# Optimization experiments

Hardware: AMD Instinct MI355X
Metric: run time of the kernel (lower is better)

## Reference

```python
import jax, jax.numpy as jnp
import numpy as np
import math

D = 512; H = 4; HD = 128; S = 100; B = 32
HIN, WIN = 143, 111
HOUT, WOUT = 135, 103
FLAT = HIN * WIN  # 15873


def _pe():
    pos = np.arange(S, dtype=np.float32)[:, None]
    div = np.exp(np.arange(0, D, 2, dtype=np.float32) * (-math.log(10000.0) / D))
    pe = np.zeros((S, D), dtype=np.float32)
    pe[:, 0::2] = np.sin(pos * div)
    pe[:, 1::2] = np.cos(pos * div)
    return jnp.asarray(pe[:, None, :])  # (S,1,D)


def _pool_mat(n_in, n_out):
    # PyTorch AdaptiveAvgPool semantics: window [floor(i*in/out), ceil((i+1)*in/out))
    M = np.zeros((n_out, n_in), dtype=np.float32)
    for i in range(n_out):
        s = (i * n_in) // n_out
        e = -((-(i + 1) * n_in) // n_out)
        M[i, s:e] = 1.0 / (e - s)
    return jnp.asarray(M)


def _ln(x, g, b, eps=1e-5):
    m = jnp.mean(x, -1, keepdims=True)
    v = jnp.mean((x - m) ** 2, -1, keepdims=True)
    return (x - m) * jax.lax.rsqrt(v + eps) * g + b


def _mha(q_in, kv_in, qkv_w, qkv_b, pw, pb, key_pad):
    # q_in: (Sq,B,D), kv_in: (Sk,B,D); seq-first like nn.Transformer
    q = q_in @ qkv_w[:D].T + qkv_b[:D]
    k = kv_in @ qkv_w[D:2 * D].T + qkv_b[D:2 * D]
    v = kv_in @ qkv_w[2 * D:].T + qkv_b[2 * D:]
    Sq, Bb = q.shape[0], q.shape[1]
    Sk = k.shape[0]
    q = q.reshape(Sq, Bb, H, HD)
    k = k.reshape(Sk, Bb, H, HD)
    v = v.reshape(Sk, Bb, H, HD)
    sc = jnp.einsum('qbhd,kbhd->bhqk', q, k) / math.sqrt(HD)
    if key_pad is not None:
        sc = jnp.where(key_pad[:, None, None, :], -1e9, sc)
    a = jax.nn.softmax(sc, -1)
    o = jnp.einsum('bhqk,kbhd->qbhd', a, v).reshape(Sq, Bb, D)
    return o @ pw.T + pb


def _forward(x, fc1_w, fc1_b, fc2_w, fc2_b, fc3_w, fc3_b,
             out1_w, out1_b, out2_w, out2_b, out3_w, out3_b,
             enc_qkv_w, enc_qkv_b, enc_proj_w, enc_proj_b,
             enc_ff1_w, enc_ff1_b, enc_ff2_w, enc_ff2_b,
             enc_ln1_g, enc_ln1_b, enc_ln2_g, enc_ln2_b, enc_lnf_g, enc_lnf_b,
             dec_sa_qkv_w, dec_sa_qkv_b, dec_sa_proj_w, dec_sa_proj_b,
             dec_ca_qkv_w, dec_ca_qkv_b, dec_ca_proj_w, dec_ca_proj_b,
             dec_ff1_w, dec_ff1_b, dec_ff2_w, dec_ff2_b,
             dec_ln1_g, dec_ln1_b, dec_ln2_g, dec_ln2_b, dec_ln3_g, dec_ln3_b,
             dec_lnf_g, dec_lnf_b):
    Bb = x.shape[0]
    # Vectorized replacement of the per-sample torch.nonzero double loop:
    # padding[b,i] = True iff all timesteps k >= i are all-zero (and i >= 1).
    nz = jnp.any(x != 0, axis=(2, 3))  # (B,S)
    suffix_any = jnp.flip(jnp.cumsum(jnp.flip(nz, 1).astype(jnp.int32), 1), 1) > 0
    padding = (~suffix_any).at[:, 0].set(False)  # torch loop never touches step 0

    h = x.reshape(Bb * S, FLAT)
    h = jax.nn.relu(h @ fc1_w.T + fc1_b)
    h = jax.nn.relu(h @ fc2_w.T + fc2_b)
    h = jax.nn.relu(h @ fc3_w.T + fc3_b)
    h = h.reshape(Bb, S, D).transpose(1, 0, 2) + _pe()  # (S,B,D)

    for i in range(2):  # encoder, post-norm
        a = _mha(h, h, enc_qkv_w[i], enc_qkv_b[i], enc_proj_w[i], enc_proj_b[i], padding)
        h = _ln(h + a, enc_ln1_g[i], enc_ln1_b[i])
        f = jax.nn.relu(h @ enc_ff1_w[i].T + enc_ff1_b[i]) @ enc_ff2_w[i].T + enc_ff2_b[i]
        h = _ln(h + f, enc_ln2_g[i], enc_ln2_b[i])
    memory = _ln(h, enc_lnf_g, enc_lnf_b)

    t = jnp.ones((1, Bb, D), jnp.float32)  # trg
    for i in range(2):  # decoder, post-norm
        a = _mha(t, t, dec_sa_qkv_w[i], dec_sa_qkv_b[i], dec_sa_proj_w[i], dec_sa_proj_b[i], None)
        t = _ln(t + a, dec_ln1_g[i], dec_ln1_b[i])
        a = _mha(t, memory, dec_ca_qkv_w[i], dec_ca_qkv_b[i], dec_ca_proj_w[i], dec_ca_proj_b[i], None)
        t = _ln(t + a, dec_ln2_g[i], dec_ln2_b[i])
        f = jax.nn.relu(t @ dec_ff1_w[i].T + dec_ff1_b[i]) @ dec_ff2_w[i].T + dec_ff2_b[i]
        t = _ln(t + f, dec_ln3_g[i], dec_ln3_b[i])
    t = _ln(t, dec_lnf_g, dec_lnf_b)

    o = t[0]  # (B,512)
    o = jax.nn.relu(o @ out1_w.T + out1_b)
    o = jax.nn.relu(o @ out2_w.T + out2_b)
    o = jax.nn.relu(o @ out3_w.T + out3_b)
    o = o.reshape(Bb, HIN, WIN)
    return jnp.einsum('oh,bhw,pw->bop', _pool_mat(HIN, HOUT), o, _pool_mat(WIN, WOUT))


def setup_inputs() -> dict:
    key = jax.random.key(0)
    it = iter(jax.random.split(key, 48))

    def w(shape):
        return jax.random.normal(next(it), shape, jnp.float32) * 0.02

    x = jax.random.normal(next(it), (B, S, HIN, WIN), jnp.float32)
    lengths = jax.random.randint(next(it), (B,), 1, S + 1)
    keep = (jnp.arange(S)[None, :] < lengths[:, None]).astype(jnp.float32)
    x = x * keep[:, :, None, None]  # ragged: trailing timesteps are all-zero

    z, o1 = jnp.zeros, jnp.ones
    return dict(
        x=x,
        fc1_w=w((4096, FLAT)), fc1_b=z(4096),
        fc2_w=w((2048, 4096)), fc2_b=z(2048),
        fc3_w=w((D, 2048)), fc3_b=z(D),
        out1_w=w((2048, D)), out1_b=z(2048),
        out2_w=w((4096, 2048)), out2_b=z(4096),
        out3_w=w((FLAT, 4096)), out3_b=z(FLAT),
        enc_qkv_w=w((2, 3 * D, D)), enc_qkv_b=z((2, 3 * D)),
        enc_proj_w=w((2, D, D)), enc_proj_b=z((2, D)),
        enc_ff1_w=w((2, 1024, D)), enc_ff1_b=z((2, 1024)),
        enc_ff2_w=w((2, D, 1024)), enc_ff2_b=z((2, D)),
        enc_ln1_g=o1((2, D)), enc_ln1_b=z((2, D)),
        enc_ln2_g=o1((2, D)), enc_ln2_b=z((2, D)),
        enc_lnf_g=o1(D), enc_lnf_b=z(D),
        dec_sa_qkv_w=w((2, 3 * D, D)), dec_sa_qkv_b=z((2, 3 * D)),
        dec_sa_proj_w=w((2, D, D)), dec_sa_proj_b=z((2, D)),
        dec_ca_qkv_w=w((2, 3 * D, D)), dec_ca_qkv_b=z((2, 3 * D)),
        dec_ca_proj_w=w((2, D, D)), dec_ca_proj_b=z((2, D)),
        dec_ff1_w=w((2, 1024, D)), dec_ff1_b=z((2, 1024)),
        dec_ff2_w=w((2, D, 1024)), dec_ff2_b=z((2, D)),
        dec_ln1_g=o1((2, D)), dec_ln1_b=z((2, D)),
        dec_ln2_g=o1((2, D)), dec_ln2_b=z((2, D)),
        dec_ln3_g=o1((2, D)), dec_ln3_b=z((2, D)),
        dec_lnf_g=o1(D), dec_lnf_b=z(D),
    )


def reference(x, fc1_w, fc1_b, fc2_w, fc2_b, fc3_w, fc3_b,
              out1_w, out1_b, out2_w, out2_b, out3_w, out3_b,
              enc_qkv_w, enc_qkv_b, enc_proj_w, enc_proj_b,
              enc_ff1_w, enc_ff1_b, enc_ff2_w, enc_ff2_b,
              enc_ln1_g, enc_ln1_b, enc_ln2_g, enc_ln2_b, enc_lnf_g, enc_lnf_b,
              dec_sa_qkv_w, dec_sa_qkv_b, dec_sa_proj_w, dec_sa_proj_b,
              dec_ca_qkv_w, dec_ca_qkv_b, dec_ca_proj_w, dec_ca_proj_b,
              dec_ff1_w, dec_ff1_b, dec_ff2_w, dec_ff2_b,
              dec_ln1_g, dec_ln1_b, dec_ln2_g, dec_ln2_b, dec_ln3_g, dec_ln3_b,
              dec_lnf_g, dec_lnf_b):
    return _forward(x, fc1_w, fc1_b, fc2_w, fc2_b, fc3_w, fc3_b,
                    out1_w, out1_b, out2_w, out2_b, out3_w, out3_b,
                    enc_qkv_w, enc_qkv_b, enc_proj_w, enc_proj_b,
                    enc_ff1_w, enc_ff1_b, enc_ff2_w, enc_ff2_b,
                    enc_ln1_g, enc_ln1_b, enc_ln2_g, enc_ln2_b, enc_lnf_g, enc_lnf_b,
                    dec_sa_qkv_w, dec_sa_qkv_b, dec_sa_proj_w, dec_sa_proj_b,
                    dec_ca_qkv_w, dec_ca_qkv_b, dec_ca_proj_w, dec_ca_proj_b,
                    dec_ff1_w, dec_ff1_b, dec_ff2_w, dec_ff2_b,
                    dec_ln1_g, dec_ln1_b, dec_ln2_g, dec_ln2_b, dec_ln3_g, dec_ln3_b,
                    dec_lnf_g, dec_lnf_b)
```

## Files before the change

kernel.cpp:

```cpp
#include <hip/hip_runtime.h>
#include <hip/hip_bf16.h>

#define SEQ   100
#define BATCH 32
#define FLATIN 15873
#define KPAD1  16384
#define ROWS   3200
#define MPAD   3328
#define NOUT3  16000

typedef __attribute__((ext_vector_type(8))) short short8;
typedef __attribute__((ext_vector_type(4))) short short4v;
typedef __attribute__((ext_vector_type(4))) float f32x4;

__device__ __forceinline__ void gload_lds16(const void* g, void* l) {
  __builtin_amdgcn_global_load_lds((const __attribute__((address_space(1))) void*)g,
                                   (__attribute__((address_space(3))) void*)l, 16, 0, 0);
}

__device__ __forceinline__ int xcd_swizzle(int id, int nwg) {
  const int q = nwg >> 3, r = nwg & 7;
  const int x = id & 7, p = id >> 3;
  return (x < r ? x * (q + 1) : r * (q + 1) + (x - r) * q) + p;
}
// ... 86 lines not shown
__global__ __launch_bounds__(256)
void gemm_direct(const __hip_bfloat16* __restrict__ A, const __hip_bfloat16* __restrict__ W,
                 const float* __restrict__ bias, float* __restrict__ Cf,
                 __hip_bfloat16* __restrict__ Cb, int K, int ldc, int mtiles)
{
  __shared__ __align__(16) short lds[16384];
  short* As = lds;
  short* Bs = lds + 8192;
  const int GATHER = 0;
  const int* idx = nullptr;
  const int wg = xcd_swizzle(blockIdx.x, gridDim.x);
  const int m0 = (wg % mtiles) << 7;
  const int n0 = (wg / mtiles) << 7;

  GEMM_BODY(0, K)

  const int fr = lane & 15, fq = lane >> 4;
#pragma unroll
  for (int j = 0; j < 4; ++j) {
    const int n = n0 + wc + (j << 4) + fr;
    const float bb = bias[n];
#pragma unroll
    for (int i = 0; i < 4; ++i)
#pragma unroll
      for (int r = 0; r < 4; ++r) {
        const int m = m0 + wr + (i << 4) + (fq << 2) + r;
        float v = acc[i][j][r] + bb;
        if (RELU) v = fmaxf(v, 0.f);
        if (OF32) Cf[(size_t)m * ldc + n] = v;
        if (OB16) Cb[(size_t)m * ldc + n] = __float2bfloat16(v);
      }
  }
}

template<int RELU, int OF32, int OB16>
__global__ __launch_bounds__(256)
void reduce_kernel(const float* __restrict__ P, size_t pstride, int ksl,
                   const float* __restrict__ bias, float* __restrict__ Cf,
                   __hip_bfloat16* __restrict__ Cb, int N,
                   const int* __restrict__ cnt)
{
  const int row = blockIdx.y;
  if (cnt) { const int cp = (cnt[0] + 127) & ~127; if (row >= cp) return; }
  const int n = (blockIdx.x * 256 + threadIdx.x) * 4;
  if (n >= N) return;
  const size_t o = (size_t)row * N + n;
  const float4 b4 = *(const float4*)(bias + n);
  float4 s = *(const float4*)(P + o);
  for (int k = 1; k < ksl; ++k) {
    const float4 p = *(const float4*)(P + (size_t)k * pstride + o);
    s.x += p.x; s.y += p.y; s.z += p.z; s.w += p.w;
  }
  s.x += b4.x; s.y += b4.y; s.z += b4.z; s.w += b4.w;
  if (RELU) {
    s.x = fmaxf(s.x, 0.f); s.y = fmaxf(s.y, 0.f);
    s.z = fmaxf(s.z, 0.f); s.w = fmaxf(s.w, 0.f);
  }
  if (OF32) *(float4*)(Cf + o) = s;
  if (OB16) {
    union { short4v v; __hip_bfloat16 h[4]; } u;
    u.h[0] = __float2bfloat16(s.x);
    u.h[1] = __float2bfloat16(s.y);
    u.h[2] = __float2bfloat16(s.z);
    u.h[3] = __float2bfloat16(s.w);
    *(short4v*)(Cb + o) = u.v;
  }
}

__global__ __launch_bounds__(256)
void conv_x_kernel(const float* __restrict__ x, __hip_bfloat16* __restrict__ xb,
                   int* __restrict__ nz)
{
  __shared__ int sred[4];
  const int m = blockIdx.x;
  const int t = threadIdx.x;
  __hip_bfloat16* dst = xb + (size_t)m * KPAD1;
  if (m == ROWS) {
    const __hip_bfloat162 z2 = {__float2bfloat16(0.f), __float2bfloat16(0.f)};
    for (int c = t; c < (KPAD1 >> 1); c += 256) *(__hip_bfloat162*)(dst + 2 * c) = z2;
    return;
  }
  const float* src = x + (size_t)m * FLATIN;
  int any = 0;
  for (int c = t; c < FLATIN; c += 256) any |= (src[c] != 0.f);
  any = __any(any) ? 1 : 0;
  if ((t & 63) == 0) sred[t >> 6] = any;
  __syncthreads();
  const int ba = sred[0] | sred[1] | sred[2] | sred[3];
  if (t == 0) nz[m] = ba;
  if (!ba) return;
  for (int c = t; c < (KPAD1 >> 1); c += 256) {
    const int c0 = 2 * c;
    const float v0 = (c0 < FLATIN) ? src[c0] : 0.f;
    const float v1 = (c0 + 1 < FLATIN) ? src[c0 + 1] : 0.f;
    __hip_bfloat162 pr;
    pr.x = __float2bfloat16(v0);
    pr.y = __float2bfloat16(v1);
    *(__hip_bfloat162*)(dst + c0) = pr;
  }
}

__global__ __launch_bounds__(256)
void compact_kernel(const int* __restrict__ nz, int* __restrict__ idx,
                    int* __restrict__ pos, int* __restrict__ cnt,
                    int* __restrict__ pad)
{
  __shared__ int wsum[4];
  __shared__ int total;
  const int t = threadIdx.x;
  int loc[13];
  int c = 0;
#pragma unroll
  for (int i = 0; i < 13; ++i) {
    const int m = t * 13 + i;
    loc[i] = (m < ROWS) ? nz[m] : 0;
    c += loc[i];
  }
  int v = c;
#pragma unroll
  for (int o = 1; o < 64; o <<= 1) {
    const int u = __shfl_up(v, o);
    if ((t & 63) >= o) v += u;
  }
  if ((t & 63) == 63) wsum[t >> 6] = v;
  __syncthreads();
  int wbase = 0;
  for (int w = 0; w < (t >> 6); ++w) wbase += wsum[w];
  int p = wbase + v - c;
#pragma unroll
  for (int i = 0; i < 13; ++i) {
    const int m = t * 13 + i;
    if (m < ROWS) {
      if (loc[i]) { idx[p] = m; pos[m] = p; ++p; }
      else pos[m] = -1;
    }
  }
  if (t == 255) total = p;
  __syncthreads();
  const int count = total;
  if (t == 0) cnt[0] = count + 1;
  for (int i = count + t; i < MPAD; i += 256) idx[i] = ROWS;
  for (int m = t; m < ROWS; m += 256) if (pos[m] < 0) pos[m] = count;
  if (t < 32) {
    int any = 0;
    for (int s = 99; s >= 0; --s) {
      any |= nz[t * 100 + s];
      pad[t * 100 + s] = (s > 0 && !any) ? 1 : 0;
    }
  }
}

__global__ __launch_bounds__(256)
void cvt_pad_kernel(const float* __restrict__ in, __hip_bfloat16* __restrict__ out,
                    int rin, int cin, int cout)
{
  const int c = (blockIdx.x * 256 + threadIdx.x) * 2;
  const int r = blockIdx.y;
  if (c >= cout) return;
  const int rv = (r < rin);
  const float v0 = (rv && c < cin) ? in[(size_t)r * cin + c] : 0.f;
  const float v1 = (rv && c + 1 < cin) ? in[(size_t)r * cin + c + 1] : 0.f;
  __hip_bfloat162 pr;
  pr.x = __float2bfloat16(v0);
  pr.y = __float2bfloat16(v1);
  *(__hip_bfloat162*)(out + (size_t)r * cout + c) = pr;
}

struct CvtArgs {
  const float* src[8];
  __hip_bfloat16* dst[8];
  int cum[8];
};
__global__ __launch_bounds__(256)
void cvt_multi_kernel(CvtArgs a)
{
  const int bid = blockIdx.x;
  int seg = 0;
#pragma unroll
  for (int i = 1; i < 8; ++i) if (bid >= a.cum[i]) seg = i;
  const size_t e0 = ((size_t)(bid - a.cum[seg]) << 11) + (threadIdx.x << 3);
  const float4 v0 = *(const float4*)(a.src[seg] + e0);
  const float4 v1 = *(const float4*)(a.src[seg] + e0 + 4);
  union { short4v v; __hip_bfloat16 h[4]; } u0, u1;
  u0.h[0] = __float2bfloat16(v0.x); u0.h[1] = __float2bfloat16(v0.y);
  u0.h[2] = __float2bfloat16(v0.z); u0.h[3] = __float2bfloat16(v0.w);
  u1.h[0] = __float2bfloat16(v1.x); u1.h[1] = __float2bfloat16(v1.y);
  u1.h[2] = __float2bfloat16(v1.z); u1.h[3] = __float2bfloat16(v1.w);
  *(short4v*)(a.dst[seg] + e0) = u0.v;
  *(short4v*)(a.dst[seg] + e0 + 4) = u1.v;
}

struct TrArgs {
  const float* src[13];
  float* dst[13];
  int R[13], C[13], cum[13];
};
__global__ __launch_bounds__(256)
void transpose_kernel(TrArgs a)
{
  __shared__ float tbuf[64][65];
  const int bid = blockIdx.x;
  int seg = 0;
#pragma unroll
  for (int i = 1; i < 13; ++i) if (bid >= a.cum[i]) seg = i;
  const int local = bid - a.cum[seg];
  const int R = a.R[seg], C = a.C[seg];
  const int tilesC = C >> 6;
  const int r0 = (local / tilesC) << 6;
  const int c0 = (local % tilesC) << 6;
  const int tx = threadIdx.x & 63, ty = threadIdx.x >> 6;
  const float* s = a.src[seg];
  float* d = a.dst[seg];
#pragma unroll
  for (int i = 0; i < 16; ++i) {
    const int rr = (ty << 4) + i;
    tbuf[rr][tx] = s[(size_t)(r0 + rr) * C + c0 + tx];
  }
  __syncthreads();
#pragma unroll
  for (int i = 0; i < 16; ++i) {
    const int cc = (ty << 4) + i;
    d[(size_t)(c0 + cc) * R + r0 + tx] = tbuf[tx][cc];
  }
}

__global__ void bias_pad_kernel(const float* __restrict__ b, float* __restrict__ bp)
{
  const int i = blockIdx.x * 256 + threadIdx.x;
  if (i < NOUT3) bp[i] = (i < FLATIN) ? b[i] : 0.f;
}

__global__ __launch_bounds__(256)
void scatter_pe_reduce(const float* __restrict__ P, size_t pstride, int ksl,
                       const int* __restrict__ pos, const float* __restrict__ bias,
                       float* __restrict__ hf, __hip_bfloat16* __restrict__ hb)
{
  const int m = blockIdx.x;
  const int s = m % 100, b = m / 100;
  const int src = pos[m];
  const int t = threadIdx.x;
  const size_t sb = (size_t)src * 512;
  const size_t db = (size_t)(s * 32 + b) * 512;
#pragma unroll
  for (int u = 0; u < 2; ++u) {
    const int d = t + u * 256;
    float v = bias[d];
    for (int k = 0; k < ksl; ++k) v += P[(size_t)k * pstride + sb + d];
    const float div = expf((float)(2 * (d >> 1)) * (-9.210340371976184f / 512.f));
    const float arg = (float)s * div;
    const float pe = (d & 1) ? cosf(arg) : sinf(arg);
    v = fmaxf(v, 0.f) + pe;
    hf[db + d] = v;
    hb[db + d] = __float2bfloat16(v);
  }
}

__global__ __launch_bounds__(256)
void ln_kernel(const float* __restrict__ x, const float* __restrict__ res,
               const float* __restrict__ g, const float* __restrict__ bta,
               const float* __restrict__ gf, const float* __restrict__ bf_,
               int dofinal, float* __restrict__ y, __hip_bfloat16* __restrict__ yb)
{
  __shared__ float rs[4], rss[4];
  const int row = blockIdx.x;
  const int t = threadIdx.x;
  const size_t base = (size_t)row * 512;
  float v0 = x[base + t];
  float v1 = x[base + t + 256];
  if (res) { v0 += res[base + t]; v1 += res[base + t + 256]; }
  float o0, o1;
#pragma unroll
  for (int pass = 0; pass < 2; ++pass) {
    float s = v0 + v1, ss = v0 * v0 + v1 * v1;
#pragma unroll
    for (int o = 32; o > 0; o >>= 1) { s += __shfl_xor(s, o); ss += __shfl_xor(ss, o); }
    if ((t & 63) == 0) { rs[t >> 6] = s; rss[t >> 6] = ss; }
    __syncthreads();
    s = rs[0] + rs[1] + rs[2] + rs[3];
    ss = rss[0] + rss[1] + rss[2] + rss[3];
    __syncthreads();
    const float mean = s * (1.f / 512.f);
    const float var = ss * (1.f / 512.f) - mean * mean;
    const float inv = rsqrtf(var + 1e-5f);
    const float* gg = (pass == 0) ? g : gf;
    const float* bb = (pass == 0) ? bta : bf_;
    o0 = (v0 - mean) * inv * gg[t] + bb[t];
    o1 = (v1 - mean) * inv * gg[t + 256] + bb[t + 256];
    if (pass == 1 || !dofinal) break;
    v0 = o0; v1 = o1;
  }
  if (y) {
    y[base + t] = o0;
    y[base + t + 256] = o1;
  }
  if (yb) {
    yb[base + t] = __float2bfloat16(o0);
    yb[base + t + 256] = __float2bfloat16(o1);
  }
}

__global__ __launch_bounds__(256)
void enc_attn_kernel(const float* __restrict__ qkv, const int* __restrict__ pad,
                     __hip_bfloat16* __restrict__ ob)
{
  __shared__ float Ks[100][129];
  __shared__ float Qs[128];
  __shared__ float Ps[100];
  __shared__ float red[4];
  const int bh = blockIdx.x;
  const int b = bh >> 2, h = bh & 3;
  const int q0 = blockIdx.y * 25;
  const int t = threadIdx.x;
// ... 16 lines not shown
      for (int d = 0; d < 128; ++d) a += Qs[d] * kr[d];
      sc = masked ? -1e9f : (a * scale);
    }
    float mx = sc;
#pragma unroll
    for (int o = 32; o > 0; o >>= 1) mx = fmaxf(mx, __shfl_xor(mx, o));
    if ((t & 63) == 0) red[t >> 6] = mx;
    __syncthreads();
    mx = fmaxf(fmaxf(red[0], red[1]), fmaxf(red[2], red[3]));
    const float e = (t < 100) ? expf(sc - mx) : 0.f;
    float sm = e;
#pragma unroll
    for (int o = 32; o > 0; o >>= 1) sm += __shfl_xor(sm, o);
    __syncthreads();
    if ((t & 63) == 0) red[t >> 6] = sm;
    __syncthreads();
    sm = red[0] + red[1] + red[2] + red[3];
    if (t < 100) Ps[t] = e;
    __syncthreads();
    if (t < 128) {
      float a = 0.f;
      const float* vb = qkv + 1024 + h * 128 + t;
      for (int k = 0; k < 100; ++k) a += Ps[k] * vb[(size_t)(k * 32 + b) * 1536];
      ob[(size_t)(q * 32 + b) * 512 + h * 128 + t] = __float2bfloat16(a / sm);
    }
  }
}

template<int N, int K, int RELU>
__device__ __forceinline__ void gemvT(int tid, const float* S,
                                      const float* __restrict__ WT,
                                      const float* __restrict__ bias,
                                      float* out, float* part)
{
  constexpr int NQ = N / 4;
  constexpr int G = 512 / NQ;
  constexpr int KP = K / G;
  const int p = tid % NQ;
  const int g = tid / NQ;
  const float4* wp = (const float4*)WT;
  float ax = 0.f, ay = 0.f, az = 0.f, aw = 0.f;
  const int kend = g * KP + KP;
#pragma unroll 8
  for (int k = g * KP; k < kend; ++k) {
    const float s = S[k];
    const float4 w = wp[(size_t)k * NQ + p];
    ax += s * w.x; ay += s * w.y; az += s * w.z; aw += s * w.w;
  }
  float4 a4 = {ax, ay, az, aw};
  *(float4*)(part + g * N + 4 * p) = a4;
  __syncthreads();
#pragma unroll
  for (int n = tid; n < N; n += 512) {
    float v = bias[n];
#pragma unroll
    for (int q = 0; q < G; ++q) v += part[q * N + n];
    if (RELU) v = fmaxf(v, 0.f);
    out[n] = v;
  }
  __syncthreads();
}

#define BLOCK_LN512(V, G, B, O)                                                 \
  {                                                                             \
    float s_ = (V), ss_ = (V) * (V);                                            \
    _Pragma("unroll")                                                           \
    for (int o_ = 32; o_ > 0; o_ >>= 1) {                                       \
      s_ += __shfl_xor(s_, o_); ss_ += __shfl_xor(ss_, o_);                     \
    }                                                                           \
    if ((tid & 63) == 0) { red[tid >> 6] = s_; red2[tid >> 6] = ss_; }          \
    __syncthreads();                                                            \
    s_ = 0.f; ss_ = 0.f;                                                        \
    _Pragma("unroll")                                                           \
    for (int w_ = 0; w_ < 8; ++w_) { s_ += red[w_]; ss_ += red2[w_]; }          \
    const float mean_ = s_ * (1.f / 512.f);                                     \
    const float inv_ = rsqrtf(ss_ * (1.f / 512.f) - mean_ * mean_ + 1e-5f);     \
    O = ((V) - mean_) * inv_ * (G)[tid] + (B)[tid];                             \
    __syncthreads();                                                            \
  }

__global__ __launch_bounds__(512)
void dec_layer(const float* __restrict__ tin,
               const float* __restrict__ kvb,
               const float* __restrict__ WvT, const float* __restrict__ bv,
               const float* __restrict__ WpT, const float* __restrict__ bp,
               const float* __restrict__ g1, const float* __restrict__ b1,
               const float* __restrict__ WqT, const float* __restrict__ bq,
               const float* __restrict__ WcpT, const float* __restrict__ bcp,
               const float* __restrict__ g2, const float* __restrict__ b2,
               const float* __restrict__ W1T, const float* __restrict__ b1f,
               const float* __restrict__ W2T, const float* __restrict__ b2f,
               const float* __restrict__ g3, const float* __restrict__ b3,
               const float* __restrict__ gf, const float* __restrict__ bf_,
               int dofinal, float* __restrict__ tout)
{
  __shared__ float Ts[512], Bs[512], Cs[512], F1[1024], part[2048];
  __shared__ float Ps[4][104];
  __shared__ float red[8], red2[8];
  const int r = blockIdx.x, tid = threadIdx.x;
  Ts[tid] = tin ? tin[r * 512 + tid] : 1.0f;
  __syncthreads();

  gemvT<512, 512, 0>(tid, Ts, WvT, bv, Bs, part);
  gemvT<512, 512, 0>(tid, Bs, WpT, bp, Cs, part);
  {
    const float rr = Cs[tid] + Ts[tid];
    float o;
    BLOCK_LN512(rr, g1, b1, o)
    Ts[tid] = o;
  }
  __syncthreads();

  gemvT<512, 512, 0>(tid, Ts, WqT, bq, Bs, part);

  if (tid < 256) {
    const int h = tid >> 6, lane = tid & 63;
    const float scale = 0.08838834764831845f;
    const float* Qh = Bs + h * 128;
    float s0, s1 = -3e38f;
    {
      const float* kr = kvb + ((size_t)(lane * 32 + r)) * 1024 + h * 128;
      float a = 0.f;
#pragma unroll 16
      for (int d = 0; d < 128; ++d) a += Qh[d] * kr[d];
      s0 = a * scale;
    }
    if (lane + 64 < 100) {
      const float* kr = kvb + ((size_t)((lane + 64) * 32 + r)) * 1024 + h * 128;
      float a = 0.f;
#pragma unroll 16
      for (int d = 0; d < 128; ++d) a += Qh[d] * kr[d];
      s1 = a * scale;
    }
    float mx = fmaxf(s0, s1);
#pragma unroll
    for (int o = 32; o > 0; o >>= 1) mx = fmaxf(mx, __shfl_xor(mx, o));
    const float e0 = expf(s0 - mx);
    const float e1 = (lane + 64 < 100) ? expf(s1 - mx) : 0.f;
    float sm = e0 + e1;
#pragma unroll
    for (int o = 32; o > 0; o >>= 1) sm += __shfl_xor(sm, o);
    Ps[h][lane] = e0 / sm;
    if (lane + 64 < 100) Ps[h][lane + 64] = e1 / sm;
  }
  __syncthreads();
  if (tid < 256) {
    const int h = tid >> 6, lane = tid & 63;
#pragma unroll
    for (int u = 0; u < 2; ++u) {
      const int d = lane + u * 64;
      const float* vb = kvb + 512 + h * 128 + d;
      float a = 0.f;
      for (int k = 0; k < 100; ++k) a += Ps[h][k] * vb[(size_t)(k * 32 + r) * 1024];
      Bs[h * 128 + d] = a;
    }
  }
  __syncthreads();

  gemvT<512, 512, 0>(tid, Bs, WcpT, bcp, Cs, part);
  {
    const float rr = Cs[tid] + Ts[tid];
    float o;
    BLOCK_LN512(rr, g2, b2, o)
    Ts[tid] = o;
  }
  __syncthreads();

  gemvT<1024, 512, 1>(tid, Ts, W1T, b1f, F1, part);
  gemvT<512, 1024, 0>(tid, F1, W2T, b2f, Cs, part);
  {
    const float rr = Cs[tid] + Ts[tid];
    float o;
    BLOCK_LN512(rr, g3, b3, o)
    if (dofinal) {
      float f;
      BLOCK_LN512(o, gf, bf_, f)
      o = f;
    }
    tout[r * 512 + tid] = o;
  }
}

__global__ __launch_bounds__(256)
void out1_kernel(const float* __restrict__ A, const float* __restrict__ WT,
                 const float* __restrict__ bias, __hip_bfloat16* __restrict__ Cb)
{
  __shared__ float S[512];
  const int r = blockIdx.x;
  const int tid = threadIdx.x;
  const int n0 = tid * 8;
  if (r >= 32) {
    const short4v z = {0, 0, 0, 0};
    *(short4v*)(Cb + (size_t)r * 2048 + n0) = z;
    *(short4v*)(Cb + (size_t)r * 2048 + n0 + 4) = z;
    return;
  }
  S[tid] = A[r * 512 + tid];
  S[tid + 256] = A[r * 512 + tid + 256];
  __syncthreads();
  float a[8] = {0.f, 0.f, 0.f, 0.f, 0.f, 0.f, 0.f, 0.f};
  const float4* wp = (const float4*)WT;
#pragma unroll 4
  for (int k = 0; k < 512; ++k) {
    const float s = S[k];
    const float4 w0 = wp[(size_t)k * 512 + tid * 2];
    const float4 w1 = wp[(size_t)k * 512 + tid * 2 + 1];
    a[0] += s * w0.x; a[1] += s * w0.y; a[2] += s * w0.z; a[3] += s * w0.w;
    a[4] += s * w1.x; a[5] += s * w1.y; a[6] += s * w1.z; a[7] += s * w1.w;
  }
  union { short4v v; __hip_bfloat16 h[4]; } u0, u1;
#pragma unroll
  for (int i = 0; i < 4; ++i) {
    u0.h[i] = __float2bfloat16(fmaxf(a[i] + bias[n0 + i], 0.f));
    u1.h[i] = __float2bfloat16(fmaxf(a[4 + i] + bias[n0 + 4 + i], 0.f));
  }
  *(short4v*)(Cb + (size_t)r * 2048 + n0) = u0.v;
  *(short4v*)(Cb + (size_t)r * 2048 + n0 + 4) = u1.v;
}

__global__ __launch_bounds__(256)
void reduce_pool(const float* __restrict__ P, size_t pstride,
                 const float* __restrict__ bias, float* __restrict__ out)
{
  __shared__ float row[NOUT3];
  const int b = blockIdx.x, t = threadIdx.x;
  for (int n = t * 4; n < NOUT3; n += 1024) {
    const size_t o = (size_t)b * NOUT3 + n;
    float4 s = *(const float4*)(P + o);
#pragma unroll
    for (int k = 1; k < 4; ++k) {
      const float4 p = *(const float4*)(P + (size_t)k * pstride + o);
      s.x += p.x; s.y += p.y; s.z += p.z; s.w += p.w;
    }
    const float4 b4 = *(const float4*)(bias + n);
    row[n]     = fmaxf(s.x + b4.x, 0.f);
    row[n + 1] = fmaxf(s.y + b4.y, 0.f);
    row[n + 2] = fmaxf(s.z + b4.z, 0.f);
    row[n + 3] = fmaxf(s.w + b4.w, 0.f);
  }
  __syncthreads();
  for (int i = t; i < 135 * 103; i += 256) {
    const int j = i % 103, r = i / 103;
    const int rs = (r * 143) / 135, re = ((r + 1) * 143 + 134) / 135;
    const int cs = (j * 111) / 103, ce = ((j + 1) * 111 + 102) / 103;
    float s = 0.f;
    for (int rr = rs; rr < re; ++rr)
      for (int cc = cs; cc < ce; ++cc)
        s += row[rr * 111 + cc];
    out[(size_t)b * (135 * 103) + i] = s / (float)((re - rs) * (ce - cs));
  }
}

extern "C" void kernel_launch(void* const* d_in, const int* in_sizes, int n_in,
                              void* d_out, int out_size, void* d_ws, size_t ws_size,
                              hipStream_t stream)
{
  (void)in_sizes; (void)n_in; (void)out_size; (void)ws_size;

  const float* x          = (const float*)d_in[0];
  const float* fc1_w      = (const float*)d_in[1];
  const float* fc1_b      = (const float*)d_in[2];
  const float* fc2_w      = (const float*)d_in[3];
  const float* fc2_b      = (const float*)d_in[4];
  const float* fc3_w      = (const float*)d_in[5];
  const float* fc3_b      = (const float*)d_in[6];
  const float* out1_w     = (const float*)d_in[7];
  const float* out1_b     = (const float*)d_in[8];
  const float* out2_w     = (const float*)d_in[9];
  const float* out2_b     = (const float*)d_in[10];
  const float* out3_w     = (const float*)d_in[11];
  const float* out3_b     = (const float*)d_in[12];
  const float* enc_qkv_w  = (const float*)d_in[13];
  const float* enc_qkv_b  = (const float*)d_in[14];
  const float* enc_proj_w = (const float*)d_in[15];
  const float* enc_proj_b = (const float*)d_in[16];
  const float* enc_ff1_w  = (const float*)d_in[17];
  const float* enc_ff1_b  = (const float*)d_in[18];
  const float* enc_ff2_w  = (const float*)d_in[19];
  const float* enc_ff2_b  = (const float*)d_in[20];
  const float* enc_ln1_g  = (const float*)d_in[21];
  const float* enc_ln1_b  = (const float*)d_in[22];
  const float* enc_ln2_g  = (const float*)d_in[23];
  const float* enc_ln2_b  = (const float*)d_in[24];
  const float* enc_lnf_g  = (const float*)d_in[25];
  const float* enc_lnf_b  = (const float*)d_in[26];
  const float* dec_sa_qkv_w  = (const float*)d_in[27];
  const float* dec_sa_qkv_b  = (const float*)d_in[28];
  const float* dec_sa_proj_w = (const float*)d_in[29];
  const float* dec_sa_proj_b = (const float*)d_in[30];
  const float* dec_ca_qkv_w  = (const float*)d_in[31];
  const float* dec_ca_qkv_b  = (const float*)d_in[32];
  const float* dec_ca_proj_w = (const float*)d_in[33];
  const float* dec_ca_proj_b = (const float*)d_in[34];
  const float* dec_ff1_w  = (const float*)d_in[35];
  const float* dec_ff1_b  = (const float*)d_in[36];
  const float* dec_ff2_w  = (const float*)d_in[37];
  const float* dec_ff2_b  = (const float*)d_in[38];
  const float* dec_ln1_g  = (const float*)d_in[39];
  const float* dec_ln1_b  = (const float*)d_in[40];
  const float* dec_ln2_g  = (const float*)d_in[41];
  const float* dec_ln2_b  = (const float*)d_in[42];
  const float* dec_ln3_g  = (const float*)d_in[43];
  const float* dec_ln3_b  = (const float*)d_in[44];
  const float* dec_lnf_g  = (const float*)d_in[45];
  const float* dec_lnf_b  = (const float*)d_in[46];

  char* wsp = (char*)d_ws;
  size_t off = 0;
  auto alloc = [&](size_t nbytes) -> char* {
    char* p = wsp + off;
    off += (nbytes + 255) & ~(size_t)255;
    return p;
  };

  __hip_bfloat16* xb     = (__hip_bfloat16*)alloc((size_t)MPAD * KPAD1 * 2);
  __hip_bfloat16* Wb1    = (__hip_bfloat16*)alloc((size_t)4096 * KPAD1 * 2);
  __hip_bfloat16* Wb2    = (__hip_bfloat16*)alloc((size_t)2048 * 4096 * 2);
  __hip_bfloat16* Wb3    = (__hip_bfloat16*)alloc((size_t)512 * 2048 * 2);
  __hip_bfloat16* Wqkvb  = (__hip_bfloat16*)alloc((size_t)2 * 1536 * 512 * 2);
  __hip_bfloat16* Wprojb = (__hip_bfloat16*)alloc((size_t)2 * 512 * 512 * 2);
  __hip_bfloat16* Wff1b  = (__hip_bfloat16*)alloc((size_t)2 * 1024 * 512 * 2);
  __hip_bfloat16* Wff2b  = (__hip_bfloat16*)alloc((size_t)2 * 512 * 1024 * 2);
  __hip_bfloat16* Wdkvb  = (__hip_bfloat16*)alloc((size_t)2 * 1536 * 512 * 2);
  int*   nz      = (int*)alloc(ROWS * 4);
  int*   padmask = (int*)alloc(ROWS * 4);
  int*   idx     = (int*)alloc(MPAD * 4);
  int*   pos     = (int*)alloc(ROWS * 4);
  int*   cnt     = (int*)alloc(256);
  __hip_bfloat16* h1c = (__hip_bfloat16*)alloc((size_t)MPAD * 4096 * 2);
  __hip_bfloat16* h2c = (__hip_bfloat16*)alloc((size_t)MPAD * 2048 * 2);
  float* hf  = (float*)alloc((size_t)ROWS * 512 * 4);
  __hip_bfloat16* hb = (__hip_bfloat16*)alloc((size_t)ROWS * 512 * 2);
  float* qkvbuf = (float*)alloc((size_t)ROWS * 1536 * 4);
  __hip_bfloat16* attnb = (__hip_bfloat16*)alloc((size_t)ROWS * 512 * 2);
  float* pjf  = (float*)alloc((size_t)ROWS * 512 * 4);
  __hip_bfloat16* f1b = (__hip_bfloat16*)alloc((size_t)ROWS * 1024 * 2);
  float* f2f  = (float*)alloc((size_t)ROWS * 512 * 4);
  float* memf = (float*)alloc((size_t)ROWS * 512 * 4);
  __hip_bfloat16* memb = (__hip_bfloat16*)alloc((size_t)ROWS * 512 * 2);
  float* kvbuf0 = (float*)alloc((size_t)ROWS * 1024 * 4);
  float* kvbuf1 = (float*)alloc((size_t)ROWS * 1024 * 4);
  float* tbuf = (float*)alloc(32 * 512 * 4);
  float* biasP = (float*)alloc(NOUT3 * 4);
  float* WvT[2]  = { (float*)alloc(512 * 512 * 4), (float*)alloc(512 * 512 * 4) };
  float* WpT[2]  = { (float*)alloc(512 * 512 * 4), (float*)alloc(512 * 512 * 4) };
  float* WqT[2]  = { (float*)alloc(512 * 512 * 4), (float*)alloc(512 * 512 * 4) };
  float* WcpT[2] = { (float*)alloc(512 * 512 * 4), (float*)alloc(512 * 512 * 4) };
  float* W1T[2]  = { (float*)alloc(512 * 1024 * 4), (float*)alloc(512 * 1024 * 4) };
  float* W2T[2]  = { (float*)alloc(1024 * 512 * 4), (float*)alloc(1024 * 512 * 4) };
  float* Wo1T    = (float*)alloc((size_t)512 * 2048 * 4);
  float* fcP  = (float*)alloc((size_t)4 * MPAD * 4096 * 4);
  float* encP = (float*)alloc((size_t)2 * ROWS * 1536 * 4);

  float* outP = fcP;
  __hip_bfloat16* Wo3b = (__hip_bfloat16*)((char*)fcP + ((size_t)48 << 20));
  __hip_bfloat16* Wo2b = (__hip_bfloat16*)encP;
  __hip_bfloat16* o1b  = (__hip_bfloat16*)((char*)encP + ((size_t)20 << 20));
  __hip_bfloat16* o2b  = (__hip_bfloat16*)((char*)encP + ((size_t)22 << 20));

  const size_t psF1 = (size_t)MPAD * 4096;
  const size_t psF2 = (size_t)MPAD * 2048;
  const size_t psF3 = (size_t)MPAD * 512;

  conv_x_kernel<<<ROWS + 1, 256, 0, stream>>>(x, xb, nz);
  compact_kernel<<<1, 256, 0, stream>>>(nz, idx, pos, cnt, padmask);
  {
    CvtArgs a;
    const float* srcs[8] = { enc_qkv_w, enc_proj_w, enc_ff1_w, enc_ff2_w,
                             dec_ca_qkv_w, fc2_w, fc3_w, out2_w };
    __hip_bfloat16* dsts[8] = { Wqkvb, Wprojb, Wff1b, Wff2b, Wdkvb, Wb2, Wb3, Wo2b };
    const int counts[8] = { 2*1536*512, 2*512*512, 2*1024*512, 2*512*1024,
                            2*1536*512, 2048*4096, 512*2048, 4096*2048 };
    int c = 0;
    for (int i = 0; i < 8; ++i) { a.src[i] = srcs[i]; a.dst[i] = dsts[i];
                                  a.cum[i] = c; c += counts[i] >> 11; }
    cvt_multi_kernel<<<c, 256, 0, stream>>>(a);
  }
  cvt_pad_kernel<<<dim3(KPAD1 / 512, 4096), 256, 0, stream>>>(fc1_w, Wb1, 4096, FLATIN, KPAD1);
  {
    TrArgs a;
    const float* srcs[13];
    float* dsts[13];
    int R[13], C[13];
    int n = 0;
    for (int L = 0; L < 2; ++L) {
      srcs[n] = dec_sa_qkv_w + (size_t)L * 1536 * 512 + (size_t)1024 * 512;
      dsts[n] = WvT[L]; R[n] = 512; C[n] = 512; ++n;
      srcs[n] = dec_sa_proj_w + (size_t)L * 512 * 512;
      dsts[n] = WpT[L]; R[n] = 512; C[n] = 512; ++n;
      srcs[n] = dec_ca_qkv_w + (size_t)L * 1536 * 512;
      dsts[n] = WqT[L]; R[n] = 512; C[n] = 512; ++n;
      srcs[n] = dec_ca_proj_w + (size_t)L * 512 * 512;
      dsts[n] = WcpT[L]; R[n] = 512; C[n] = 512; ++n;
      srcs[n] = dec_ff1_w + (size_t)L * 1024 * 512;
      dsts[n] = W1T[L]; R[n] = 1024; C[n] = 512; ++n;
      srcs[n] = dec_ff2_w + (size_t)L * 512 * 1024;
      dsts[n] = W2T[L]; R[n] = 512; C[n] = 1024; ++n;
    }
    srcs[n] = out1_w; dsts[n] = Wo1T; R[n] = 2048; C[n] = 512; ++n;
    int c = 0;
    for (int i = 0; i < 13; ++i) {
      a.src[i] = srcs[i]; a.dst[i] = dsts[i]; a.R[i] = R[i]; a.C[i] = C[i];
      a.cum[i] = c; c += (R[i] >> 6) * (C[i] >> 6);
    }
    transpose_kernel<<<c, 256, 0, stream>>>(a);
  }

  gemm_bf16<1><<<26 * 32 * 2, 256, 0, stream>>>(xb, Wb1, idx, cnt, fcP,
      KPAD1, 4096, 26, 2, psF1);
  reduce_kernel<1, 0, 1><<<dim3(4, MPAD), 256, 0, stream>>>(fcP, psF1, 2,
      fc1_b, nullptr, h1c, 4096, cnt);
  gemm_bf16<0><<<26 * 16 * 2, 256, 0, stream>>>(h1c, Wb2, nullptr, cnt, fcP,
      4096, 2048, 26, 2, psF2);
  reduce_kernel<1, 0, 1><<<dim3(2, MPAD), 256, 0, stream>>>(fcP, psF2, 2,
      fc2_b, nullptr, h2c, 2048, cnt);
  gemm_bf16<0><<<26 * 4 * 4, 256, 0, stream>>>(h2c, Wb3, nullptr, cnt, fcP,
      2048, 512, 26, 4, psF3);
  scatter_pe_reduce<<<ROWS, 256, 0, stream>>>(fcP, psF3, 4, pos, fc3_b, hf, hb);

  for (int L = 0; L < 2; ++L) {
    gemm_direct<0, 1, 0><<<25 * 12, 256, 0, stream>>>(hb, Wqkvb + (size_t)L * 1536 * 512,
        enc_qkv_b + L * 1536, qkvbuf, nullptr, 512, 1536, 25);
    enc_attn_kernel<<<dim3(128, 4), 256, 0, stream>>>(qkvbuf, padmask, attnb);
    gemm_direct<0, 1, 0><<<25 * 4, 256, 0, stream>>>(attnb, Wprojb + (size_t)L * 512 * 512,
        enc_proj_b + L * 512, pjf, nullptr, 512, 512, 25);
    ln_kernel<<<ROWS, 256, 0, stream>>>(hf, pjf, enc_ln1_g + L * 512, enc_ln1_b + L * 512,
        nullptr, nullptr, 0, hf, hb);
    gemm_direct<1, 0, 1><<<25 * 8, 256, 0, stream>>>(hb, Wff1b + (size_t)L * 1024 * 512,
        enc_ff1_b + L * 1024, nullptr, f1b, 512, 1024, 25);
    gemm_direct<0, 1, 0><<<25 * 4, 256, 0, stream>>>(f1b, Wff2b + (size_t)L * 512 * 1024,
        enc_ff2_b + L * 512, f2f, nullptr, 1024, 512, 25);
    if (L == 0) {
      ln_kernel<<<ROWS, 256, 0, stream>>>(hf, f2f, enc_ln2_g, enc_ln2_b,
          nullptr, nullptr, 0, hf, hb);
    } else {
      ln_kernel<<<ROWS, 256, 0, stream>>>(hf, f2f, enc_ln2_g + 512, enc_ln2_b + 512,
          enc_lnf_g, enc_lnf_b, 1, memf, memb);
    }
  }

  gemm_direct<0, 1, 0><<<25 * 8, 256, 0, stream>>>(memb, Wdkvb + (size_t)512 * 512,
      dec_ca_qkv_b + 512, kvbuf0, nullptr, 512, 1024, 25);
  gemm_direct<0, 1, 0><<<25 * 8, 256, 0, stream>>>(memb, Wdkvb + ((size_t)1536 + 512) * 512,
      dec_ca_qkv_b + 1536 + 512, kvbuf1, nullptr, 512, 1024, 25);

  for (int L = 0; L < 2; ++L) {
    dec_layer<<<32, 512, 0, stream>>>(
        (L == 0) ? nullptr : tbuf,
        (L == 0) ? kvbuf0 : kvbuf1,
        WvT[L], dec_sa_qkv_b + L * 1536 + 1024,
        WpT[L], dec_sa_proj_b + L * 512,
        dec_ln1_g + L * 512, dec_ln1_b + L * 512,
        WqT[L], dec_ca_qkv_b + L * 1536,
        WcpT[L], dec_ca_proj_b + L * 512,
        dec_ln2_g + L * 512, dec_ln2_b + L * 512,
        W1T[L], dec_ff1_b + L * 1024,
        W2T[L], dec_ff2_b + L * 512,
        dec_ln3_g + L * 512, dec_ln3_b + L * 512,
        dec_lnf_g, dec_lnf_b, (L == 1) ? 1 : 0, tbuf);
  }

  out1_kernel<<<128, 256, 0, stream>>>(tbuf, Wo1T, out1_b, o1b);
  cvt_pad_kernel<<<dim3(8, NOUT3), 256, 0, stream>>>(out3_w, Wo3b, FLATIN, 4096, 4096);
  bias_pad_kernel<<<(NOUT3 + 255) / 256, 256, 0, stream>>>(out3_b, biasP);

  gemm_bf16<0><<<32 * 4, 256, 0, stream>>>(o1b, Wo2b, nullptr, nullptr, outP,
      2048, 4096, 1, 4, (size_t)128 * 4096);
  reduce_kernel<1, 0, 1><<<dim3(4, 128), 256, 0, stream>>>(outP, (size_t)128 * 4096, 4,
      out2_b, nullptr, o2b, 4096, nullptr);
  gemm_bf16<0><<<125 * 4, 256, 0, stream>>>(o2b, Wo3b, nullptr, nullptr, outP,
      4096, NOUT3, 1, 4, (size_t)128 * NOUT3);
  reduce_pool<<<32, 256, 0, stream>>>(outP, (size_t)128 * NOUT3, biasP, (float*)d_out);

  (void)qkvbuf; (void)pjf; (void)f2f; (void)memf;
}
```

Baseline: 1.539 ms.

## Fuse small kernels, merge decoder KV GEMMs, raise fc2 split-K

Several unrelated changes. The zero-row check in conv_x is folded into the conversion loop, so the input is read once, but all-zero rows are now also converted. The two decoder cross-attention KV GEMMs become one GEMM with a concatenated weight and a bias packed in compact_kernel. out1 is fused into the last dec_layer, the bias_pad kernel is dropped in favour of a bounds check in reduce_pool, and fc2's split-K goes from 2 to 4. This removes launches and redundant passes, at the cost of more partial-sum traffic for fc2 and an out1 projection limited to 32 blocks.

```diff
diff --git a/kernel.cpp b/kernel.cpp
--- a/kernel.cpp
+++ b/kernel.cpp
@@ -192,28 +192,27 @@
   }
   const float* src = x + (size_t)m * FLATIN;
   int any = 0;
-  for (int c = t; c < FLATIN; c += 256) any |= (src[c] != 0.f);
-  any = __any(any) ? 1 : 0;
-  if ((t & 63) == 0) sred[t >> 6] = any;
-  __syncthreads();
-  const int ba = sred[0] | sred[1] | sred[2] | sred[3];
-  if (t == 0) nz[m] = ba;
-  if (!ba) return;
   for (int c = t; c < (KPAD1 >> 1); c += 256) {
     const int c0 = 2 * c;
     const float v0 = (c0 < FLATIN) ? src[c0] : 0.f;
     const float v1 = (c0 + 1 < FLATIN) ? src[c0 + 1] : 0.f;
+    any |= (v0 != 0.f) | (v1 != 0.f);
     __hip_bfloat162 pr;
     pr.x = __float2bfloat16(v0);
     pr.y = __float2bfloat16(v1);
     *(__hip_bfloat162*)(dst + c0) = pr;
   }
+  any = __any(any) ? 1 : 0;
+  if ((t & 63) == 0) sred[t >> 6] = any;
+  __syncthreads();
+  if (t == 0) nz[m] = sred[0] | sred[1] | sred[2] | sred[3];
 }
 
 __global__ __launch_bounds__(256)
 void compact_kernel(const int* __restrict__ nz, int* __restrict__ idx,
                     int* __restrict__ pos, int* __restrict__ cnt,
-                    int* __restrict__ pad)
+                    int* __restrict__ pad,
+                    const float* __restrict__ dkvb, float* __restrict__ kvbias)
 {
   __shared__ int wsum[4];
   __shared__ int total;
@@ -257,6 +256,11 @@
       any |= nz[t * 100 + s];
       pad[t * 100 + s] = (s > 0 && !any) ? 1 : 0;
     }
+  }
+#pragma unroll
+  for (int i = t; i < 2048; i += 256) {
+    const int L = i >> 10, j = i & 1023;
+    kvbias[i] = dkvb[L * 1536 + 512 + j];
   }
 }
 
@@ -277,9 +281,9 @@
 }
 
 struct CvtArgs {
-  const float* src[8];
-  __hip_bfloat16* dst[8];
-  int cum[8];
+  const float* src[9];
+  __hip_bfloat16* dst[9];
+  int cum[9];
 };
 __global__ __launch_bounds__(256)
 void cvt_multi_kernel(CvtArgs a)
@@ -287,7 +291,7 @@
   const int bid = blockIdx.x;
   int seg = 0;
 #pragma unroll
-  for (int i = 1; i < 8; ++i) if (bid >= a.cum[i]) seg = i;
+  for (int i = 1; i < 9; ++i) if (bid >= a.cum[i]) seg = i;
   const size_t e0 = ((size_t)(bid - a.cum[seg]) << 11) + (threadIdx.x << 3);
   const float4 v0 = *(const float4*)(a.src[seg] + e0);
   const float4 v1 = *(const float4*)(a.src[seg] + e0 + 4);
@@ -332,12 +336,6 @@
     const int cc = (ty << 4) + i;
     d[(size_t)(c0 + cc) * R + r0 + tx] = tbuf[tx][cc];
   }
-}
-
-__global__ void bias_pad_kernel(const float* __restrict__ b, float* __restrict__ bp)
-{
-  const int i = blockIdx.x * 256 + threadIdx.x;
-  if (i < NOUT3) bp[i] = (i < FLATIN) ? b[i] : 0.f;
 }
 
 __global__ __launch_bounds__(256)
@@ -520,6 +518,7 @@
 __global__ __launch_bounds__(512)
 void dec_layer(const float* __restrict__ tin,
                const float* __restrict__ kvb,
+               int kvstride,
                const float* __restrict__ WvT, const float* __restrict__ bv,
                const float* __restrict__ WpT, const float* __restrict__ bp,
                const float* __restrict__ g1, const float* __restrict__ b1,
@@ -530,7 +529,9 @@
                const float* __restrict__ W2T, const float* __restrict__ b2f,
                const float* __restrict__ g3, const float* __restrict__ b3,
                const float* __restrict__ gf, const float* __restrict__ bf_,
-               int dofinal, float* __restrict__ tout)
+               int dofinal, float* __restrict__ tout,
+               const float* __restrict__ Wo1T, const float* __restrict__ ob1,
+               __hip_bfloat16* __restrict__ o1b)
 {
   __shared__ float Ts[512], Bs[512], Cs[512], F1[1024], part[2048];
   __shared__ float Ps[4][104];
@@ -557,14 +558,14 @@
     const float* Qh = Bs + h * 128;
     float s0, s1 = -3e38f;
     {
-      const float* kr = kvb + ((size_t)(lane * 32 + r)) * 1024 + h * 128;
+      const float* kr = kvb + (size_t)(lane * 32 + r) * kvstride + h * 128;
       float a = 0.f;
 #pragma unroll 16
       for (int d = 0; d < 128; ++d) a += Qh[d] * kr[d];
       s0 = a * scale;
     }
     if (lane + 64 < 100) {
-      const float* kr = kvb + ((size_t)((lane + 64) * 32 + r)) * 1024 + h * 128;
+      const float* kr = kvb + (size_t)((lane + 64) * 32 + r) * kvstride + h * 128;
       float a = 0.f;
 #pragma unroll 16
       for (int d = 0; d < 128; ++d) a += Qh[d] * kr[d];
@@ -589,7 +590,7 @@
       const int d = lane + u * 64;
       const float* vb = kvb + 512 + h * 128 + d;
       float a = 0.f;
-      for (int k = 0; k < 100; ++k) a += Ps[h][k] * vb[(size_t)(k * 32 + r) * 1024];
+      for (int k = 0; k < 100; ++k) a += Ps[h][k] * vb[(size_t)(k * 32 + r) * kvstride];
       Bs[h * 128 + d] = a;
     }
   }
@@ -616,44 +617,29 @@
       o = f;
     }
     tout[r * 512 + tid] = o;
-  }
-}
-
-__global__ __launch_bounds__(256)
-void out1_kernel(const float* __restrict__ A, const float* __restrict__ WT,
-                 const float* __restrict__ bias, __hip_bfloat16* __restrict__ Cb)
-{
-  __shared__ float S[512];
-  const int r = blockIdx.x;
-  const int tid = threadIdx.x;
-  const int n0 = tid * 8;
-  if (r >= 32) {
-    const short4v z = {0, 0, 0, 0};
-    *(short4v*)(Cb + (size_t)r * 2048 + n0) = z;
-    *(short4v*)(Cb + (size_t)r * 2048 + n0 + 4) = z;
-    return;
-  }
-  S[tid] = A[r * 512 + tid];
-  S[tid + 256] = A[r * 512 + tid + 256];
-  __syncthreads();
-  float a[8] = {0.f, 0.f, 0.f, 0.f, 0.f, 0.f, 0.f, 0.f};
-  const float4* wp = (const float4*)WT;
-#pragma unroll 4
-  for (int k = 0; k < 512; ++k) {
-    const float s = S[k];
-    const float4 w0 = wp[(size_t)k * 512 + tid * 2];
-    const float4 w1 = wp[(size_t)k * 512 + tid * 2 + 1];
-    a[0] += s * w0.x; a[1] += s * w0.y; a[2] += s * w0.z; a[3] += s * w0.w;
-    a[4] += s * w1.x; a[5] += s * w1.y; a[6] += s * w1.z; a[7] += s * w1.w;
-  }
-  union { short4v v; __hip_bfloat16 h[4]; } u0, u1;
-#pragma unroll
-  for (int i = 0; i < 4; ++i) {
-    u0.h[i] = __float2bfloat16(fmaxf(a[i] + bias[n0 + i], 0.f));
-    u1.h[i] = __float2bfloat16(fmaxf(a[4 + i] + bias[n0 + 4 + i], 0.f));
-  }
-  *(short4v*)(Cb + (size_t)r * 2048 + n0) = u0.v;
-  *(short4v*)(Cb + (size_t)r * 2048 + n0 + 4) = u1.v;
+    if (dofinal) {
+      Ts[tid] = o;
+      __syncthreads();
+      const float4* wp = (const float4*)Wo1T;
+      float ax = 0.f, ay = 0.f, az = 0.f, aw = 0.f;
+#pragma unroll 8
+      for (int k = 0; k < 512; ++k) {
+        const float s = Ts[k];
+        const float4 w = wp[(size_t)k * 512 + tid];
+        ax += s * w.x; ay += s * w.y; az += s * w.z; aw += s * w.w;
+      }
+      union { short4v v; __hip_bfloat16 h[4]; } u;
+      u.h[0] = __float2bfloat16(fmaxf(ax + ob1[4 * tid], 0.f));
+      u.h[1] = __float2bfloat16(fmaxf(ay + ob1[4 * tid + 1], 0.f));
+      u.h[2] = __float2bfloat16(fmaxf(az + ob1[4 * tid + 2], 0.f));
+      u.h[3] = __float2bfloat16(fmaxf(aw + ob1[4 * tid + 3], 0.f));
+      *(short4v*)(o1b + (size_t)r * 2048 + 4 * tid) = u.v;
+      const short4v z = {0, 0, 0, 0};
+#pragma unroll
+      for (int rr = r + 32; rr < 128; rr += 32)
+        *(short4v*)(o1b + (size_t)rr * 2048 + 4 * tid) = z;
+    }
+  }
 }
 
 __global__ __launch_bounds__(256)
@@ -670,11 +656,10 @@
       const float4 p = *(const float4*)(P + (size_t)k * pstride + o);
       s.x += p.x; s.y += p.y; s.z += p.z; s.w += p.w;
     }
-    const float4 b4 = *(const float4*)(bias + n);
-    row[n]     = fmaxf(s.x + b4.x, 0.f);
-    row[n + 1] = fmaxf(s.y + b4.y, 0.f);
-    row[n + 2] = fmaxf(s.z + b4.z, 0.f);
-    row[n + 3] = fmaxf(s.w + b4.w, 0.f);
+    row[n]     = fmaxf(s.x + ((n     < FLATIN) ? bias[n]     : 0.f), 0.f);
+    row[n + 1] = fmaxf(s.y + ((n + 1 < FLATIN) ? bias[n + 1] : 0.f), 0.f);
+    row[n + 2] = fmaxf(s.z + ((n + 2 < FLATIN) ? bias[n + 2] : 0.f), 0.f);
+    row[n + 3] = fmaxf(s.w + ((n + 3 < FLATIN) ? bias[n + 3] : 0.f), 0.f);
   }
   __syncthreads();
   for (int i = t; i < 135 * 103; i += 256) {
@@ -759,12 +744,13 @@
   __hip_bfloat16* Wprojb = (__hip_bfloat16*)alloc((size_t)2 * 512 * 512 * 2);
   __hip_bfloat16* Wff1b  = (__hip_bfloat16*)alloc((size_t)2 * 1024 * 512 * 2);
   __hip_bfloat16* Wff2b  = (__hip_bfloat16*)alloc((size_t)2 * 512 * 1024 * 2);
-  __hip_bfloat16* Wdkvb  = (__hip_bfloat16*)alloc((size_t)2 * 1536 * 512 * 2);
+  __hip_bfloat16* Wkv2b  = (__hip_bfloat16*)alloc((size_t)2048 * 512 * 2);
   int*   nz      = (int*)alloc(ROWS * 4);
   int*   padmask = (int*)alloc(ROWS * 4);
   int*   idx     = (int*)alloc(MPAD * 4);
   int*   pos     = (int*)alloc(ROWS * 4);
   int*   cnt     = (int*)alloc(256);
+  float* kvbias  = (float*)alloc(2048 * 4);
   __hip_bfloat16* h1c = (__hip_bfloat16*)alloc((size_t)MPAD * 4096 * 2);
   __hip_bfloat16* h2c = (__hip_bfloat16*)alloc((size_t)MPAD * 2048 * 2);
   float* hf  = (float*)alloc((size_t)ROWS * 512 * 4);
@@ -774,12 +760,9 @@
   float* pjf  = (float*)alloc((size_t)ROWS * 512 * 4);
   __hip_bfloat16* f1b = (__hip_bfloat16*)alloc((size_t)ROWS * 1024 * 2);
   float* f2f  = (float*)alloc((size_t)ROWS * 512 * 4);
-  float* memf = (float*)alloc((size_t)ROWS * 512 * 4);
   __hip_bfloat16* memb = (__hip_bfloat16*)alloc((size_t)ROWS * 512 * 2);
-  float* kvbuf0 = (float*)alloc((size_t)ROWS * 1024 * 4);
-  float* kvbuf1 = (float*)alloc((size_t)ROWS * 1024 * 4);
+  float* kv01 = (float*)alloc((size_t)ROWS * 2048 * 4);
   float* tbuf = (float*)alloc(32 * 512 * 4);
-  float* biasP = (float*)alloc(NOUT3 * 4);
   float* WvT[2]  = { (float*)alloc(512 * 512 * 4), (float*)alloc(512 * 512 * 4) };
   float* WpT[2]  = { (float*)alloc(512 * 512 * 4), (float*)alloc(512 * 512 * 4) };
   float* WqT[2]  = { (float*)alloc(512 * 512 * 4), (float*)alloc(512 * 512 * 4) };
@@ -801,16 +784,21 @@
   const size_t psF3 = (size_t)MPAD * 512;
 
   conv_x_kernel<<<ROWS + 1, 256, 0, stream>>>(x, xb, nz);
-  compact_kernel<<<1, 256, 0, stream>>>(nz, idx, pos, cnt, padmask);
+  compact_kernel<<<1, 256, 0, stream>>>(nz, idx, pos, cnt, padmask,
+                                        dec_ca_qkv_b, kvbias);
   {
     CvtArgs a;
-    const float* srcs[8] = { enc_qkv_w, enc_proj_w, enc_ff1_w, enc_ff2_w,
-                             dec_ca_qkv_w, fc2_w, fc3_w, out2_w };
-    __hip_bfloat16* dsts[8] = { Wqkvb, Wprojb, Wff1b, Wff2b, Wdkvb, Wb2, Wb3, Wo2b };
-    const int counts[8] = { 2*1536*512, 2*512*512, 2*1024*512, 2*512*1024,
-                            2*1536*512, 2048*4096, 512*2048, 4096*2048 };
+    const float* srcs[9] = { enc_qkv_w, enc_proj_w, enc_ff1_w, enc_ff2_w,
+                             dec_ca_qkv_w + (size_t)512 * 512,
+                             dec_ca_qkv_w + (size_t)(1536 + 512) * 512,
+                             fc2_w, fc3_w, out2_w };
+    __hip_bfloat16* dsts[9] = { Wqkvb, Wprojb, Wff1b, Wff2b,
+                                Wkv2b, Wkv2b + (size_t)1024 * 512,
+                                Wb2, Wb3, Wo2b };
+    const int counts[9] = { 2*1536*512, 2*512*512, 2*1024*512, 2*512*1024,
+                            1024*512, 1024*512, 2048*4096, 512*2048, 4096*2048 };
     int c = 0;
-    for (int i = 0; i < 8; ++i) { a.src[i] = srcs[i]; a.dst[i] = dsts[i];
+    for (int i = 0; i < 9; ++i) { a.src[i] = srcs[i]; a.dst[i] = dsts[i];
                                   a.cum[i] = c; c += counts[i] >> 11; }
     cvt_multi_kernel<<<c, 256, 0, stream>>>(a);
   }
@@ -848,9 +836,9 @@
       KPAD1, 4096, 26, 2, psF1);
   reduce_kernel<1, 0, 1><<<dim3(4, MPAD), 256, 0, stream>>>(fcP, psF1, 2,
       fc1_b, nullptr, h1c, 4096, cnt);
-  gemm_bf16<0><<<26 * 16 * 2, 256, 0, stream>>>(h1c, Wb2, nullptr, cnt, fcP,
-      4096, 2048, 26, 2, psF2);
-  reduce_kernel<1, 0, 1><<<dim3(2, MPAD), 256, 0, stream>>>(fcP, psF2, 2,
+  gemm_bf16<0><<<26 * 16 * 4, 256, 0, stream>>>(h1c, Wb2, nullptr, cnt, fcP,
+      4096, 2048, 26, 4, psF2);
+  reduce_kernel<1, 0, 1><<<dim3(2, MPAD), 256, 0, stream>>>(fcP, psF2, 4,
       fc2_b, nullptr, h2c, 2048, cnt);
   gemm_bf16<0><<<26 * 4 * 4, 256, 0, stream>>>(h2c, Wb3, nullptr, cnt, fcP,
       2048, 512, 26, 4, psF3);
@@ -873,19 +861,17 @@
           nullptr, nullptr, 0, hf, hb);
     } else {
       ln_kernel<<<ROWS, 256, 0, stream>>>(hf, f2f, enc_ln2_g + 512, enc_ln2_b + 512,
-          enc_lnf_g, enc_lnf_b, 1, memf, memb);
-    }
-  }
-
-  gemm_direct<0, 1, 0><<<25 * 8, 256, 0, stream>>>(memb, Wdkvb + (size_t)512 * 512,
-      dec_ca_qkv_b + 512, kvbuf0, nullptr, 512, 1024, 25);
-  gemm_direct<0, 1, 0><<<25 * 8, 256, 0, stream>>>(memb, Wdkvb + ((size_t)1536 + 512) * 512,
-      dec_ca_qkv_b + 1536 + 512, kvbuf1, nullptr, 512, 1024, 25);
+          enc_lnf_g, enc_lnf_b, 1, nullptr, memb);
+    }
+  }
+
+  gemm_direct<0, 1, 0><<<25 * 16, 256, 0, stream>>>(memb, Wkv2b, kvbias,
+      kv01, nullptr, 512, 2048, 25);
 
   for (int L = 0; L < 2; ++L) {
     dec_layer<<<32, 512, 0, stream>>>(
         (L == 0) ? nullptr : tbuf,
-        (L == 0) ? kvbuf0 : kvbuf1,
+        kv01 + (size_t)L * 1024, 2048,
         WvT[L], dec_sa_qkv_b + L * 1536 + 1024,
         WpT[L], dec_sa_proj_b + L * 512,
         dec_ln1_g + L * 512, dec_ln1_b + L * 512,
@@ -895,12 +881,11 @@
         W1T[L], dec_ff1_b + L * 1024,
         W2T[L], dec_ff2_b + L * 512,
         dec_ln3_g + L * 512, dec_ln3_b + L * 512,
-        dec_lnf_g, dec_lnf_b, (L == 1) ? 1 : 0, tbuf);
-  }
-
-  out1_kernel<<<128, 256, 0, stream>>>(tbuf, Wo1T, out1_b, o1b);
+        dec_lnf_g, dec_lnf_b, (L == 1) ? 1 : 0, tbuf,
+        Wo1T, out1_b, o1b);
+  }
+
   cvt_pad_kernel<<<dim3(8, NOUT3), 256, 0, stream>>>(out3_w, Wo3b, FLATIN, 4096, 4096);
-  bias_pad_kernel<<<(NOUT3 + 255) / 256, 256, 0, stream>>>(out3_b, biasP);
 
   gemm_bf16<0><<<32 * 4, 256, 0, stream>>>(o1b, Wo2b, nullptr, nullptr, outP,
       2048, 4096, 1, 4, (size_t)128 * 4096);
@@ -908,7 +893,7 @@
       out2_b, nullptr, o2b, 4096, nullptr);
   gemm_bf16<0><<<125 * 4, 256, 0, stream>>>(o2b, Wo3b, nullptr, nullptr, outP,
       4096, NOUT3, 1, 4, (size_t)128 * NOUT3);
-  reduce_pool<<<32, 256, 0, stream>>>(outP, (size_t)128 * NOUT3, biasP, (float*)d_out);
-
-  (void)qkvbuf; (void)pjf; (void)f2f; (void)memf;
-}
+  reduce_pool<<<32, 256, 0, stream>>>(outP, (size_t)128 * NOUT3, out3_b, (float*)d_out);
+
+  (void)qkvbuf; (void)pjf; (void)f2f;
+}
```

After: 1.498 ms. 2.7% less time.
